# Kernel tuning notes

Measured on AMD Instinct MI355X. Metric: run time of the kernel, lower is better.

The kernel has to match this reference:

```python
import jax, jax.numpy as jnp
import numpy as np

N_NODES = 50000
N_EDGES = 800000
LATENT = 128
N_CENTERS = 100

def shifted_softplus(x):
    # softplus(x) - log(2), the standard (G)SchNet activation
    return jax.nn.softplus(x) - jnp.log(2.0).astype(x.dtype)

def setup_inputs() -> dict:
    key = jax.random.key(0)
    k_n, k_s, k_r, k_w1, k_w2 = jax.random.split(key, 5)
    nodes = jax.random.normal(k_n, (N_NODES, 3), dtype=jnp.float32) * 3.0  # 3D positions
    senders = jax.random.randint(k_s, (N_EDGES,), 0, N_NODES)
    receivers = jax.random.randint(k_r, (N_EDGES,), 0, N_NODES)
    # hk.nets.MLP default truncated-normal init ~ 1/sqrt(fan_in)
    W1 = jax.random.normal(k_w1, (N_CENTERS, LATENT), dtype=jnp.float32) / np.sqrt(N_CENTERS)
    b1 = jnp.zeros((LATENT,), dtype=jnp.float32)
    W2 = jax.random.normal(k_w2, (LATENT, LATENT), dtype=jnp.float32) / np.sqrt(LATENT)
    b2 = jnp.zeros((LATENT,), dtype=jnp.float32)
    return {"nodes": nodes, "senders": senders, "receivers": receivers,
            "W1": W1, "b1": b1, "W2": W2, "b2": b2}

def reference(nodes, senders, receivers, W1, b1, W2, b2):
    # Gather endpoint positions per edge and compute scalar distance
    diff = nodes[senders] - nodes[receivers]            # [E, 3]
    dist = jnp.linalg.norm(diff, axis=-1)               # [E]
    # Gaussian RBF embedding: 100 centers in [0, 10], gamma = 1.0
    centers = jnp.linspace(0.0, 10.0, N_CENTERS).astype(dist.dtype)  # [100]
    rbf = jnp.exp(-jnp.square(dist[:, None] - centers[None, :]))     # [E, 100]
    # 2-layer MLP: activation between layers only (activate_final=False)
    h = shifted_softplus(rbf @ W1 + b1)                 # [E, latent]
    out = h @ W2 + b2                                   # [E, latent]
    return out
```

## Files before the change

### kernel.cpp

```cpp
#include <hip/hip_runtime.h>
#include <hip/hip_fp16.h>
#include <math.h>


#define N_NODES_C   50000
#define N_EDGES_C   800000
#define LATENT_C    128
#define N_CENTERS_C 100
#define TABK        1024
#define DMAX        16.0f
#define LN2F        0.69314718056f

typedef float  v4f __attribute__((ext_vector_type(4)));
typedef _Float16 h4 __attribute__((ext_vector_type(4)));

__device__ __forceinline__ float shifted_softplus(float x) {
    return fmaxf(x, 0.0f) + log1pf(expf(-fabsf(x))) - LN2F;
}

__global__ void build_table_kernel(const float* __restrict__ W1, const float* __restrict__ b1,
                                   const float* __restrict__ W2, const float* __restrict__ b2,
                                   _Float16* __restrict__ table) {
    __shared__ float rbf[N_CENTERS_C];
    __shared__ float hbuf[LATENT_C];
    const int j = threadIdx.x;
    const float d = (float)blockIdx.x * (DMAX / (float)TABK);

    if (j < N_CENTERS_C) {
        const float c = (float)j * (10.0f / 99.0f);
        const float x = d - c;
        rbf[j] = expf(-x * x);
    }
    __syncthreads();

    float a = b1[j];
    #pragma unroll 4
    for (int c = 0; c < N_CENTERS_C; ++c)
        a = fmaf(rbf[c], W1[c * LATENT_C + j], a);
    hbuf[j] = shifted_softplus(a);
    __syncthreads();

    float o = b2[j];
    #pragma unroll 4
    for (int i = 0; i < LATENT_C; ++i)
        o = fmaf(hbuf[i], W2[i * LATENT_C + j], o);

    table[(size_t)blockIdx.x * LATENT_C + j] = (_Float16)o;
}

__global__ void edge_write_kernel(const float* __restrict__ nodes,
                                  const int* __restrict__ senders,
                                  const int* __restrict__ receivers,
                                  const _Float16* __restrict__ table,
                                  float* __restrict__ out) {
    const int lane = threadIdx.x & 63;
    const int half = lane >> 5;
    const int li   = lane & 31;
    const int wid  = (blockIdx.x * blockDim.x + threadIdx.x) >> 6;
    const int base = wid * 64;

    const int e = base + lane;
    const int s = senders[e];
    const int r = receivers[e];
    const float dx = nodes[3 * s + 0] - nodes[3 * r + 0];
    const float dy = nodes[3 * s + 1] - nodes[3 * r + 1];
    const float dz = nodes[3 * s + 2] - nodes[3 * r + 2];
    const float dist = sqrtf(fmaf(dx, dx, fmaf(dy, dy, dz * dz)));
    const float t = fminf(dist * ((float)TABK / DMAX), (float)TABK - 0.5f);

    #pragma unroll 4
    for (int i = 0; i < 16; ++i) {
        const int eb = base + 4 * i;
        const float t0 = __shfl(t, 4 * i + half, 64);
        const float t1 = __shfl(t, 4 * i + 2 + half, 64);
        const int   k0 = (int)t0;  const float f0 = t0 - (float)k0;
        const int   k1 = (int)t1;  const float f1 = t1 - (float)k1;

        const h4* p0 = (const h4*)(table + (size_t)k0 * LATENT_C);
        const h4* p1 = (const h4*)(table + (size_t)k1 * LATENT_C);
        const h4 a0 = p0[li], b0 = p0[li + 32];
        const h4 a1 = p1[li], b1 = p1[li + 32];

        v4f o0, o1;
        #pragma unroll
        for (int c = 0; c < 4; ++c) {
            const float A0 = (float)a0[c], B0 = (float)b0[c];
            const float A1 = (float)a1[c], B1 = (float)b1[c];
            o0[c] = fmaf(f0, B0 - A0, A0);
            o1[c] = fmaf(f1, B1 - A1, A1);
        }

        v4f* po0 = (v4f*)(out + (size_t)eb * LATENT_C);
        v4f* po1 = (v4f*)(out + (size_t)(eb + 2) * LATENT_C);
        __builtin_nontemporal_store(o0, &po0[lane]);
        __builtin_nontemporal_store(o1, &po1[lane]);
    }
}

__global__ void edge_direct_kernel(const float* __restrict__ nodes,
                                   const int* __restrict__ senders,
                                   const int* __restrict__ receivers,
                                   const float* __restrict__ W1, const float* __restrict__ b1,
                                   const float* __restrict__ W2, const float* __restrict__ b2,
                                   float* __restrict__ out) {
    __shared__ float rbf[N_CENTERS_C];
    __shared__ float hbuf[LATENT_C];
    const int j = threadIdx.x;

    for (int e = blockIdx.x; e < N_EDGES_C; e += gridDim.x) {
        const int s = senders[e];
        const int r = receivers[e];
        const float dx = nodes[3 * s + 0] - nodes[3 * r + 0];
        const float dy = nodes[3 * s + 1] - nodes[3 * r + 1];
        const float dz = nodes[3 * s + 2] - nodes[3 * r + 2];
        const float dist = sqrtf(fmaf(dx, dx, fmaf(dy, dy, dz * dz)));

        if (j < N_CENTERS_C) {
            const float c = (float)j * (10.0f / 99.0f);
            const float x = dist - c;
            rbf[j] = expf(-x * x);
        }
        __syncthreads();

        float a = b1[j];
        #pragma unroll 4
        for (int c = 0; c < N_CENTERS_C; ++c)
            a = fmaf(rbf[c], W1[c * LATENT_C + j], a);
        hbuf[j] = shifted_softplus(a);
        __syncthreads();

        float o = b2[j];
        #pragma unroll 4
        for (int i = 0; i < LATENT_C; ++i)
            o = fmaf(hbuf[i], W2[i * LATENT_C + j], o);
        out[(size_t)e * LATENT_C + j] = o;

        __syncthreads();
    }
}

extern "C" void kernel_launch(void* const* d_in, const int* in_sizes, int n_in,
                              void* d_out, int out_size, void* d_ws, size_t ws_size,
                              hipStream_t stream) {
    const float* nodes     = (const float*)d_in[0];
    const int*   senders   = (const int*)  d_in[1];
    const int*   receivers = (const int*)  d_in[2];
    const float* W1        = (const float*)d_in[3];
    const float* b1        = (const float*)d_in[4];
    const float* W2        = (const float*)d_in[5];
    const float* b2        = (const float*)d_in[6];
    float*       out       = (float*)d_out;

    const size_t table_bytes = (size_t)(TABK + 1) * LATENT_C * sizeof(_Float16);

    if (ws_size >= table_bytes) {
        _Float16* table = (_Float16*)d_ws;

        build_table_kernel<<<TABK + 1, LATENT_C, 0, stream>>>(W1, b1, W2, b2, table);
        edge_write_kernel<<<3125, 256, 0, stream>>>(nodes, senders, receivers, table, out);
    } else {
        edge_direct_kernel<<<16384, LATENT_C, 0, stream>>>(nodes, senders, receivers,
                                                           W1, b1, W2, b2, out);
    }
}
```

Measured before the change: 84.89 us.

## Fuse table build and edge write into one cooperative persistent kernel

Merges the table-building kernel and the edge interpolation/write kernel into a single cooperative launch with a grid-wide barrier between the phases. The edge phase becomes a persistent grid-stride loop over 64-edge units. This removes one kernel launch and the gap between the two kernels. In exchange it pays for a grid sync and an occupancy query on the host, and caps the grid size, so the edge phase gets less parallelism than the old 3125-block launch.

```diff
diff --git a/kernel.cpp b/kernel.cpp
--- a/kernel.cpp
+++ b/kernel.cpp
@@ -1,6 +1,9 @@
 #include <hip/hip_runtime.h>
+#include <hip/hip_cooperative_groups.h>
 #include <hip/hip_fp16.h>
 #include <math.h>
+
+namespace cg = cooperative_groups;
 
 
 #define N_NODES_C   50000
@@ -10,6 +13,7 @@
 #define TABK        1024
 #define DMAX        16.0f
 #define LN2F        0.69314718056f
+#define NWAVEUNITS  (N_EDGES_C / 64)
 
 typedef float  v4f __attribute__((ext_vector_type(4)));
 typedef _Float16 h4 __attribute__((ext_vector_type(4)));
@@ -18,14 +22,14 @@
     return fmaxf(x, 0.0f) + log1pf(expf(-fabsf(x))) - LN2F;
 }
 
-__global__ void build_table_kernel(const float* __restrict__ W1, const float* __restrict__ b1,
-                                   const float* __restrict__ W2, const float* __restrict__ b2,
-                                   _Float16* __restrict__ table) {
-    __shared__ float rbf[N_CENTERS_C];
-    __shared__ float hbuf[LATENT_C];
-    const int j = threadIdx.x;
-    const float d = (float)blockIdx.x * (DMAX / (float)TABK);
-
+__device__ __forceinline__ void build_row(const float* __restrict__ W1,
+                                          const float* __restrict__ b1,
+                                          const float* __restrict__ W2,
+                                          const float* __restrict__ b2,
+                                          _Float16* __restrict__ table,
+                                          float* rbf, float* hbuf,
+                                          int j, int row, bool active) {
+    const float d = (float)row * (DMAX / (float)TABK);
     if (j < N_CENTERS_C) {
         const float c = (float)j * (10.0f / 99.0f);
         const float x = d - c;
@@ -45,7 +49,83 @@
     for (int i = 0; i < LATENT_C; ++i)
         o = fmaf(hbuf[i], W2[i * LATENT_C + j], o);
 
-    table[(size_t)blockIdx.x * LATENT_C + j] = (_Float16)o;
+    if (active) table[(size_t)row * LATENT_C + j] = (_Float16)o;
+    __syncthreads();
+}
+
+__global__ void fused_kernel(const float* __restrict__ nodes,
+                             const int* __restrict__ senders,
+                             const int* __restrict__ receivers,
+                             const float* __restrict__ W1, const float* __restrict__ b1,
+                             const float* __restrict__ W2, const float* __restrict__ b2,
+                             _Float16* __restrict__ table,
+                             float* __restrict__ out) {
+    {
+        __shared__ float rbf[2][N_CENTERS_C];
+        __shared__ float hbuf[2][LATENT_C];
+        const int sub = threadIdx.x >> 7;
+        const int j   = threadIdx.x & 127;
+        for (int r0 = blockIdx.x * 2; r0 <= TABK; r0 += gridDim.x * 2) {
+            const int row = r0 + sub;
+            build_row(W1, b1, W2, b2, table, rbf[sub], hbuf[sub], j, row, row <= TABK);
+        }
+    }
+    cg::this_grid().sync();
+
+    const int lane = threadIdx.x & 63;
+    const int half = lane >> 5;
+    const int li   = lane & 31;
+    const int wid  = (blockIdx.x * blockDim.x + threadIdx.x) >> 6;
+    const int nw   = (gridDim.x * blockDim.x) >> 6;
+
+    for (int w = wid; w < NWAVEUNITS; w += nw) {
+        const int base = w * 64;
+
+        const int e = base + lane;
+        const int s = senders[e];
+        const int r = receivers[e];
+        const float dx = nodes[3 * s + 0] - nodes[3 * r + 0];
+        const float dy = nodes[3 * s + 1] - nodes[3 * r + 1];
+        const float dz = nodes[3 * s + 2] - nodes[3 * r + 2];
+        const float dist = sqrtf(fmaf(dx, dx, fmaf(dy, dy, dz * dz)));
+        const float t = fminf(dist * ((float)TABK / DMAX), (float)TABK - 0.5f);
+
+        #pragma unroll 4
+        for (int i = 0; i < 16; ++i) {
+            const int eb = base + 4 * i;
+            const float t0 = __shfl(t, 4 * i + half, 64);
+            const float t1 = __shfl(t, 4 * i + 2 + half, 64);
+            const int   k0 = (int)t0;  const float f0 = t0 - (float)k0;
+            const int   k1 = (int)t1;  const float f1 = t1 - (float)k1;
+
+            const h4* p0 = (const h4*)(table + (size_t)k0 * LATENT_C);
+            const h4* p1 = (const h4*)(table + (size_t)k1 * LATENT_C);
+            const h4 a0 = p0[li], b0 = p0[li + 32];
+            const h4 a1 = p1[li], b1 = p1[li + 32];
+
+            v4f o0, o1;
+            #pragma unroll
+            for (int c = 0; c < 4; ++c) {
+                const float A0 = (float)a0[c], B0 = (float)b0[c];
+                const float A1 = (float)a1[c], B1 = (float)b1[c];
+                o0[c] = fmaf(f0, B0 - A0, A0);
+                o1[c] = fmaf(f1, B1 - A1, A1);
+            }
+
+            v4f* po0 = (v4f*)(out + (size_t)eb * LATENT_C);
+            v4f* po1 = (v4f*)(out + (size_t)(eb + 2) * LATENT_C);
+            __builtin_nontemporal_store(o0, &po0[lane]);
+            __builtin_nontemporal_store(o1, &po1[lane]);
+        }
+    }
+}
+
+__global__ void build_table_kernel(const float* __restrict__ W1, const float* __restrict__ b1,
+                                   const float* __restrict__ W2, const float* __restrict__ b2,
+                                   _Float16* __restrict__ table) {
+    __shared__ float rbf[N_CENTERS_C];
+    __shared__ float hbuf[LATENT_C];
+    build_row(W1, b1, W2, b2, table, rbf, hbuf, threadIdx.x, blockIdx.x, true);
 }
 
 __global__ void edge_write_kernel(const float* __restrict__ nodes,
@@ -153,13 +233,32 @@
 
     const size_t table_bytes = (size_t)(TABK + 1) * LATENT_C * sizeof(_Float16);
 
-    if (ws_size >= table_bytes) {
-        _Float16* table = (_Float16*)d_ws;
-
-        build_table_kernel<<<TABK + 1, LATENT_C, 0, stream>>>(W1, b1, W2, b2, table);
-        edge_write_kernel<<<3125, 256, 0, stream>>>(nodes, senders, receivers, table, out);
-    } else {
+    if (ws_size < table_bytes) {
         edge_direct_kernel<<<16384, LATENT_C, 0, stream>>>(nodes, senders, receivers,
                                                            W1, b1, W2, b2, out);
-    }
-}
+        return;
+    }
+
+    _Float16* table = (_Float16*)d_ws;
+
+    int blocksPerCU = 0;
+    hipError_t oerr = hipOccupancyMaxActiveBlocksPerMultiprocessor(
+        &blocksPerCU, fused_kernel, 256, 0);
+    int grid = 1024;
+    if (oerr == hipSuccess && blocksPerCU >= 1) {
+        grid = blocksPerCU * 256;
+        if (grid > 2048) grid = 2048;
+    }
+
+    void* args[] = {(void*)&nodes, (void*)&senders, (void*)&receivers,
+                    (void*)&W1, (void*)&b1, (void*)&W2, (void*)&b2,
+                    (void*)&table, (void*)&out};
+    hipError_t lerr = hipLaunchCooperativeKernel((const void*)fused_kernel,
+                                                 dim3(grid), dim3(256),
+                                                 args, 0, stream);
+    if (lerr != hipSuccess) {
+        build_table_kernel<<<TABK + 1, LATENT_C, 0, stream>>>(W1, b1, W2, b2, table);
+        edge_write_kernel<<<NWAVEUNITS / 4, 256, 0, stream>>>(nodes, senders, receivers,
+                                                              table, out);
+    }
+}
```

New measurement: 155.2 us. 1.83x slower.
